# Performance work log

Hardware: AMD Instinct MI355X
Metric: run time of the kernel (lower is better)

## Reference

```python
import jax, jax.numpy as jnp
import numpy as np
from jax import lax

B, T, D = 4, 4096, 1024
H = 16                 # n_heads
HD = D // H            # head_dim = 64
NS = 64                # num_slots
SPH = NS // H          # slots_per_head = 4
KPH = 2                # effective per-head top_k = min(max(2, 32//16), 4) = 2
K = KPH * H            # total topk width = 32
HM = 4096              # hidden_mlp


def _p(key, shape, scale=0.02):
    return jax.random.normal(key, shape, dtype=jnp.float32) * scale


def setup_inputs() -> dict:
    key = jax.random.key(0)
    ks = jax.random.split(key, 24)
    return {
        "x": jax.random.normal(ks[0], (B, T, D), dtype=jnp.float32),
        "slot_init": _p(ks[1], (H, SPH, HD)),
        # route_mlp: Linear(2D, D) -> GELU -> Linear(D, NS); weights stored [in, out]
        "rw1": _p(ks[2], (2 * D, D)), "rb1": jnp.zeros((D,), jnp.float32),
        "rw2": _p(ks[3], (D, NS)), "rb2": jnp.zeros((NS,), jnp.float32),
        # GRUCell(HD, HD): torch layout [3*HD, HD]
        "gwi": _p(ks[4], (3 * HD, HD), 0.1), "gwh": _p(ks[5], (3 * HD, HD), 0.1),
        "gbi": jnp.zeros((3 * HD,), jnp.float32), "gbh": jnp.zeros((3 * HD,), jnp.float32),
        # slot_hidden_proj: Linear(HD, 4*HD); slot_out_head: Linear(4*HD, HD)
        "hpw": _p(ks[6], (HD, 4 * HD)), "hpb": jnp.zeros((4 * HD,), jnp.float32),
        "ohw": _p(ks[7], (4 * HD, HD)), "ohb": jnp.zeros((HD,), jnp.float32),
        # slot_value_proj: Linear(D, HM); slot_value_out: Linear(HM, D)
        "vpw": _p(ks[8], (D, HM)), "vpb": jnp.zeros((HM,), jnp.float32),
        "vow": _p(ks[9], (HM, D)), "vob": jnp.zeros((D,), jnp.float32),
        # out_proj: Linear(D, D)
        "opw": _p(ks[10], (D, D)), "opb": jnp.zeros((D,), jnp.float32),
        "tau": jnp.ones((1,), jnp.float32),
    }


def _gelu(x):
    return jax.nn.gelu(x, approximate=False)


def _forward(x, slot_init, rw1, rb1, rw2, rb2, gwi, gwh, gbi, gbh,
             hpw, hpb, ohw, ohb, vpw, vpb, vow, vob, opw, opb, tau):
    # ---- routing ----
    S0 = slot_init.reshape(NS, HD)                     # [NS, HD]
    slot_mean = S0.mean(axis=0)                        # [HD]
    slot_mean_full = jnp.tile(slot_mean, H)            # [D]
    ctx = jnp.concatenate(
        [x, jnp.broadcast_to(slot_mean_full, (B, T, D))], axis=-1)  # [B,T,2D]
    h1 = _gelu(ctx @ rw1 + rb1)
    route_logits = (h1 @ rw2 + rb2) / (jnp.abs(tau[0]) + 0.1)       # [B,T,NS]

    topk_vals, topk_idx = lax.top_k(route_logits, K)   # [B,T,K]
    topk_w = jax.nn.softmax(topk_vals, axis=-1)
    bi = jnp.arange(B)[:, None, None]
    ti = jnp.arange(T)[None, :, None]
    alpha = jnp.zeros((B, T, NS), x.dtype).at[bi, ti, topk_idx].set(topk_w)

    # ---- per-head slot pooling (vectorized over heads) ----
    alpha_h = alpha.reshape(B, T, H, SPH)              # [B,T,H,S]
    x_heads = x.reshape(B, T, H, HD)                   # [B,T,H,HD]
    slot_input = jnp.einsum('bths,bthd->bhsd', alpha_h, x_heads)   # [B,H,S,HD]
    wsum = alpha_h.sum(axis=1) + 1e-8                  # [B,H,S]
    slot_in = slot_input / wsum[..., None]

    # ---- GRU cell update (torch GRUCell semantics) ----
    h_prev = jnp.broadcast_to(slot_init[None], (B, H, SPH, HD))
    gi = slot_in @ gwi.T + gbi                         # [B,H,S,3HD]
    gh = h_prev @ gwh.T + gbh
    ir, iz, in_ = jnp.split(gi, 3, axis=-1)
    hr, hz, hn = jnp.split(gh, 3, axis=-1)
    r = jax.nn.sigmoid(ir + hr)
    z = jax.nn.sigmoid(iz + hz)
    n = jnp.tanh(in_ + r * hn)
    h_new = (1.0 - z) * n + z * h_prev                 # [B,H,S,HD]

    S_new = _gelu(h_new @ hpw + hpb) @ ohw + ohb       # [B,H,S,HD]

    # ---- broadcast back to tokens ----
    out = jnp.einsum('bths,bhsd->bthd', alpha_h, S_new).reshape(B, T, D)
    out = _gelu(out @ vpw + vpb) @ vow + vob
    out = out @ opw + opb
    return out


def reference(x, slot_init, rw1, rb1, rw2, rb2, gwi, gwh, gbi, gbh,
              hpw, hpb, ohw, ohb, vpw, vpb, vow, vob, opw, opb, tau):
    return _forward(x, slot_init, rw1, rb1, rw2, rb2, gwi, gwh, gbi, gbh,
                    hpw, hpb, ohw, ohb, vpw, vpb, vow, vob, opw, opb, tau)
```

## Files before the change

### kernel.cpp

```cpp
#include <hip/hip_runtime.h>
#include <cstddef>
#include <cstdint>

#define Bb 4
#define Tt 4096
#define Dd 1024
#define Hh 16
#define HDd 64
#define NSs 64
#define SPHh 4
#define HMm 4096
#define MTOK (Bb*Tt)

typedef _Float16 f16x8 __attribute__((ext_vector_type(8)));
typedef _Float16 f16x4 __attribute__((ext_vector_type(4)));
typedef float f32x4 __attribute__((ext_vector_type(4)));

__device__ __forceinline__ float gelu_f(float x) {
    return 0.5f * x * (1.0f + erff(x * 0.70710678118654752440f));
}

__device__ __forceinline__ int xcd_swz(int nwg) {
    int orig = blockIdx.y * gridDim.x + blockIdx.x;
    int cpx = nwg >> 3;
    return (orig & 7) * cpx + (orig >> 3);
}

__global__ __launch_bounds__(256) void cb_part_k(const float* __restrict__ slot_init,
                                                 const float* __restrict__ rw1,
                                                 float* __restrict__ cbp) {
    __shared__ float sm[64];
    int tid = threadIdx.x;
    if (tid < 64) {
        float s = 0.f;
        for (int i = 0; i < 64; ++i) s += slot_init[i * 64 + tid];
        sm[tid] = s * (1.0f / 64.0f);
    }
    __syncthreads();
    int j = blockIdx.x * 256 + tid;
    int k0 = blockIdx.y * 64;
    float acc = 0.f;
#pragma unroll 8
    for (int k = 0; k < 64; ++k)
        acc = fmaf(sm[k], rw1[(size_t)(1024 + k0 + k) * 1024 + j], acc);
    cbp[(size_t)blockIdx.y * 1024 + j] = acc;
}

__global__ __launch_bounds__(256) void cb_comb_k(const float* __restrict__ cbp,
                                                 float* __restrict__ cb) {
    int j = blockIdx.x * 256 + threadIdx.x;
    float acc = 0.f;
#pragma unroll
    for (int c = 0; c < 16; ++c) acc += cbp[(size_t)c * 1024 + j];
    cb[j] = acc;
}

__global__ __launch_bounds__(256) void wsplitT_k(const float* __restrict__ rw1,
                                                 _Float16* __restrict__ whiT,
                                                 _Float16* __restrict__ wloT) {
    __shared__ float t[32][33];
    int n0 = blockIdx.x * 32, k0 = blockIdx.y * 32;
    int tx = threadIdx.x & 31, ty = threadIdx.x >> 5;
#pragma unroll
    for (int i = 0; i < 32; i += 8)
        t[ty + i][tx] = rw1[(size_t)(k0 + ty + i) * 1024 + n0 + tx];
    __syncthreads();
#pragma unroll
    for (int i = 0; i < 32; i += 8) {
        float v = t[tx][ty + i];
        _Float16 h = (_Float16)v;
        _Float16 l = (_Float16)(v - (float)h);
        whiT[(size_t)(n0 + ty + i) * 1024 + k0 + tx] = h;
        wloT[(size_t)(n0 + ty + i) * 1024 + k0 + tx] = l;
    }
}

__global__ __launch_bounds__(256) void xsplit_k(const float* __restrict__ x,
                                                _Float16* __restrict__ xhi,
                                                _Float16* __restrict__ xlo) {
    size_t i = ((size_t)blockIdx.x * 256 + threadIdx.x) * 8;
    float4 a = *(const float4*)(x + i);
    float4 b = *(const float4*)(x + i + 4);
    float v[8] = {a.x, a.y, a.z, a.w, b.x, b.y, b.z, b.w};
    f16x8 h, l;
#pragma unroll
    for (int j = 0; j < 8; ++j) {
        _Float16 hv = (_Float16)v[j];
        h[j] = hv;
        l[j] = (_Float16)(v[j] - (float)hv);
    }
    *(f16x8*)(xhi + i) = h;
    *(f16x8*)(xlo + i) = l;
}

__global__ __launch_bounds__(512, 2) void hgemm4p_k(const _Float16* __restrict__ Ah,
                                                    const _Float16* __restrict__ Al,
                                                    const _Float16* __restrict__ Bh,
                                                    const _Float16* __restrict__ Bl,
                                                    const float* __restrict__ bias1,
                                                    const float* __restrict__ bias2,
                                                    float* __restrict__ C,
                                                    int M, int N, int K) {
    __shared__ __align__(16) _Float16 Ahs[2][256][32];
    __shared__ __align__(16) _Float16 Als[2][256][32];
    __shared__ __align__(16) _Float16 Bhs[2][256][32];
    __shared__ __align__(16) _Float16 Bls[2][256][32];
    const int tid = threadIdx.x;
    const int wid = tid >> 6;
    const int lane = tid & 63;
    const int swz = xcd_swz(gridDim.x * gridDim.y);
    const int brow = (swz / gridDim.x) * 256;
    const int bcol = (swz % gridDim.x) * 256;
    const int wm = wid >> 2;
    const int wn = wid & 3;

    const int srow = lane >> 2;
    const int scol = ((lane & 3) ^ ((lane >> 3) & 3)) * 8;
    const int fr = lane & 15;
    const int fkp = (((lane >> 4) ^ ((lane >> 1) & 3))) * 8;
    const int crow = (lane >> 4) * 4;

    const int nk = K >> 5;

    f32x4 acc[8][4];
#pragma unroll
    for (int m = 0; m < 8; ++m)
#pragma unroll
        for (int n = 0; n < 4; ++n)
            acc[m][n] = f32x4{0.f, 0.f, 0.f, 0.f};

    auto stage = [&](int t) {
        const int slot = t & 1;
        const size_t kk = (size_t)t << 5;
#pragma unroll
        for (int i = 0; i < 2; ++i) {
            int r0 = wid * 32 + i * 16;
            const _Float16* gah = Ah + (size_t)(brow + r0 + srow) * K + kk + scol;
            __builtin_amdgcn_global_load_lds(
                (const __attribute__((address_space(1))) void*)gah,
                (__attribute__((address_space(3))) void*)&Ahs[slot][r0][0], 16, 0, 0);
            const _Float16* gal = Al + (size_t)(brow + r0 + srow) * K + kk + scol;
            __builtin_amdgcn_global_load_lds(
                (const __attribute__((address_space(1))) void*)gal,
                (__attribute__((address_space(3))) void*)&Als[slot][r0][0], 16, 0, 0);
            const _Float16* gbh = Bh + (size_t)(bcol + r0 + srow) * K + kk + scol;
            __builtin_amdgcn_global_load_lds(
                (const __attribute__((address_space(1))) void*)gbh,
                (__attribute__((address_space(3))) void*)&Bhs[slot][r0][0], 16, 0, 0);
            const _Float16* gbl = Bl + (size_t)(bcol + r0 + srow) * K + kk + scol;
            __builtin_amdgcn_global_load_lds(
                (const __attribute__((address_space(1))) void*)gbl,
                (__attribute__((address_space(3))) void*)&Bls[slot][r0][0], 16, 0, 0);
        }
    };

    stage(0);
    if (nk > 1) stage(1);

    for (int t = 0; t < nk; ++t) {
        if (t + 1 < nk) asm volatile("s_waitcnt vmcnt(8)" ::: "memory");
        else            asm volatile("s_waitcnt vmcnt(0)" ::: "memory");
        __builtin_amdgcn_sched_barrier(0);
        __builtin_amdgcn_s_barrier();
        __builtin_amdgcn_sched_barrier(0);

        const int slot = t & 1;
        f16x8 afh[8], afl[8], bfh[4], bfl[4];
#pragma unroll
        for (int m = 0; m < 4; ++m) {
            afh[m] = *(const f16x8*)&Ahs[slot][wm * 128 + m * 16 + fr][fkp];
            afl[m] = *(const f16x8*)&Als[slot][wm * 128 + m * 16 + fr][fkp];
        }
#pragma unroll
        for (int n = 0; n < 4; ++n) {
            bfh[n] = *(const f16x8*)&Bhs[slot][wn * 64 + n * 16 + fr][fkp];
            bfl[n] = *(const f16x8*)&Bls[slot][wn * 64 + n * 16 + fr][fkp];
        }
        __builtin_amdgcn_sched_barrier(0);
        __builtin_amdgcn_s_barrier();
        asm volatile("s_waitcnt lgkmcnt(0)" ::: "memory");
        __builtin_amdgcn_sched_barrier(0);
        __builtin_amdgcn_s_setprio(1);
#pragma unroll
        for (int m = 0; m < 4; ++m)
#pragma unroll
            for (int n = 0; n < 4; ++n) {
                acc[m][n] = __builtin_amdgcn_mfma_f32_16x16x32_f16(afl[m], bfh[n], acc[m][n], 0, 0, 0);
                acc[m][n] = __builtin_amdgcn_mfma_f32_16x16x32_f16(afh[m], bfl[n], acc[m][n], 0, 0, 0);
                acc[m][n] = __builtin_amdgcn_mfma_f32_16x16x32_f16(afh[m], bfh[n], acc[m][n], 0, 0, 0);
            }
        __builtin_amdgcn_s_setprio(0);
        __builtin_amdgcn_sched_barrier(0);
#pragma unroll
        for (int m = 4; m < 8; ++m) {
            afh[m] = *(const f16x8*)&Ahs[slot][wm * 128 + m * 16 + fr][fkp];
            afl[m] = *(const f16x8*)&Als[slot][wm * 128 + m * 16 + fr][fkp];
        }
        asm volatile("s_waitcnt lgkmcnt(0)" ::: "memory");
        __builtin_amdgcn_sched_barrier(0);
        __builtin_amdgcn_s_barrier();
        __builtin_amdgcn_sched_barrier(0);
        if (t + 2 < nk) stage(t + 2);
        __builtin_amdgcn_s_setprio(1);
#pragma unroll
        for (int m = 4; m < 8; ++m)
#pragma unroll
            for (int n = 0; n < 4; ++n) {
                acc[m][n] = __builtin_amdgcn_mfma_f32_16x16x32_f16(afl[m], bfh[n], acc[m][n], 0, 0, 0);
                acc[m][n] = __builtin_amdgcn_mfma_f32_16x16x32_f16(afh[m], bfl[n], acc[m][n], 0, 0, 0);
                acc[m][n] = __builtin_amdgcn_mfma_f32_16x16x32_f16(afh[m], bfh[n], acc[m][n], 0, 0, 0);
            }
        __builtin_amdgcn_s_setprio(0);
        __builtin_amdgcn_sched_barrier(0);
    }

#pragma unroll
    for (int m = 0; m < 8; ++m) {
        int row0 = brow + wm * 128 + m * 16 + crow;
#pragma unroll
        for (int n = 0; n < 4; ++n) {
            int col = bcol + wn * 64 + n * 16 + fr;
            float bv = bias1[col] + bias2[col];
#pragma unroll
            for (int r = 0; r < 4; ++r) {
                float v = acc[m][n][r] + bv;
                C[(size_t)(row0 + r) * N + col] = gelu_f(v);
            }
        }
    }
    (void)M;
}

__global__ __launch_bounds__(256) void logits2_k(const float* __restrict__ A,
                                                 const float* __restrict__ Bw,
                                                 const float* __restrict__ rb2,
                                                 const float* __restrict__ taup,
                                                 float* __restrict__ Cl) {
    __shared__ float At[16][68];
    __shared__ float Bs[16][64];
    const int tid = threadIdx.x;
    const int m0 = blockIdx.x * 64;
    const int rg = tid >> 4;
    const int cg = tid & 15;
    const int srow = tid >> 2;
    const int skk  = (tid & 3) * 4;
    const int bk = tid >> 4;
    const int bc = (tid & 15) * 4;

    float acc[4][4] = {};

    for (int k0 = 0; k0 < 1024; k0 += 16) {
        float4 av = *(const float4*)(A + (size_t)(m0 + srow) * 1024 + k0 + skk);
        float4 bv = *(const float4*)(Bw + (size_t)(k0 + bk) * 64 + bc);
        __syncthreads();
        At[skk + 0][srow] = av.x;
        At[skk + 1][srow] = av.y;
        At[skk + 2][srow] = av.z;
        At[skk + 3][srow] = av.w;
        *(float4*)&Bs[bk][bc] = bv;
        __syncthreads();
#pragma unroll
        for (int k = 0; k < 16; ++k) {
            float4 a4 = *(const float4*)&At[k][rg * 4];
            float4 b4 = *(const float4*)&Bs[k][cg * 4];
            float a[4] = {a4.x, a4.y, a4.z, a4.w};
            float b[4] = {b4.x, b4.y, b4.z, b4.w};
#pragma unroll
            for (int i = 0; i < 4; ++i)
#pragma unroll
                for (int j = 0; j < 4; ++j)
                    acc[i][j] = fmaf(a[i], b[j], acc[i][j]);
        }
    }
    float inv = 1.0f / (fabsf(taup[0]) + 0.1f);
#pragma unroll
    for (int i = 0; i < 4; ++i)
#pragma unroll
        for (int j = 0; j < 4; ++j)
            Cl[(size_t)(m0 + rg * 4 + i) * 64 + cg * 4 + j] =
                (acc[i][j] + rb2[cg * 4 + j]) * inv;
}

__global__ __launch_bounds__(256) void topk_k(const float* __restrict__ logits,
                                              float* __restrict__ alpha,
                                              _Float16* __restrict__ alpha16) {
    int wave = threadIdx.x >> 6;
    int lane = threadIdx.x & 63;
    int t = blockIdx.x * 4 + wave;
    float li = logits[(size_t)t * 64 + lane];
    float m = li;
#pragma unroll
    for (int off = 32; off; off >>= 1) m = fmaxf(m, __shfl_xor(m, off, 64));
    int cnt = 0;
    for (int off = 1; off < 64; ++off) {
        int j = (lane + off) & 63;
        float lj = __shfl(li, j, 64);
        cnt += (lj > li) || (lj == li && j < lane);
    }
    float e = (cnt < 32) ? expf(li - m) : 0.0f;
    float s = e;
#pragma unroll
    for (int off = 32; off; off >>= 1) s += __shfl_xor(s, off, 64);
    float a = e / s;
    alpha[(size_t)t * 64 + lane] = a;
    alpha16[(size_t)t * 64 + lane] = (_Float16)a;
}

__global__ __launch_bounds__(256) void pool_part_k(const float* __restrict__ x,
                                                   const float* __restrict__ alpha,
                                                   float* __restrict__ part,
                                                   float* __restrict__ partw) {
    int bh = blockIdx.x;
    int c = blockIdx.y;
    int b = bh >> 4, h = bh & 15;
    int tid = threadIdx.x;
    int s = tid >> 6, d = tid & 63;
    __shared__ float lx[16][64];
    __shared__ float la[16][4];
    float acc = 0.f, wacc = 0.f;
    const int tchunk = Tt / 8;
    const int t0base = c * tchunk;
    for (int t0 = 0; t0 < tchunk; t0 += 16) {
        int ttr = tid >> 4;
        int ddr = (tid & 15) * 4;
        size_t trow = (size_t)b * Tt + t0base + t0 + ttr;
        float4 xv = *(const float4*)(x + trow * Dd + h * 64 + ddr);
        *(float4*)&lx[ttr][ddr] = xv;
        if (tid < 64) {
            int tt2 = tid >> 2, ss = tid & 3;
            la[tt2][ss] = alpha[((size_t)b * Tt + t0base + t0 + tt2) * 64 + h * 4 + ss];
        }
        __syncthreads();
#pragma unroll
        for (int q = 0; q < 16; ++q) {
            float av = la[q][s];
            acc = fmaf(av, lx[q][d], acc);
            wacc += av;
        }
        __syncthreads();
    }
    part[(((size_t)c * 64 + bh) * 4 + s) * 64 + d] = acc;
    if (d == 0) partw[((size_t)c * 64 + bh) * 4 + s] = wacc;
}

__global__ __launch_bounds__(256) void pool_comb_k(const float* __restrict__ part,
                                                   const float* __restrict__ partw,
                                                   float* __restrict__ slot_in) {
    int bh = blockIdx.x;
    int tid = threadIdx.x;
    int s = tid >> 6, d = tid & 63;
    float acc = 0.f, w = 0.f;
    for (int c = 0; c < 8; ++c) {
        acc += part[(((size_t)c * 64 + bh) * 4 + s) * 64 + d];
        w   += partw[((size_t)c * 64 + bh) * 4 + s];
    }
    slot_in[((size_t)bh * 4 + s) * 64 + d] = acc / (w + 1e-8f);
}

__global__ __launch_bounds__(64) void gru_k(const float* __restrict__ slot_in,
                                            const float* __restrict__ slot_init,
                                            const float* __restrict__ gwi,
                                            const float* __restrict__ gwh,
                                            const float* __restrict__ gbi,
                                            const float* __restrict__ gbh,
                                            const float* __restrict__ hpw,
                                            const float* __restrict__ hpb,
                                            const float* __restrict__ ohw,
                                            const float* __restrict__ ohb,
                                            float* __restrict__ S_new) {
    int slot = blockIdx.x;
    int hs = slot & 63;
    int d = threadIdx.x;
    __shared__ float si[64], hp[64], hn[64], g[256];
    si[d] = slot_in[(size_t)slot * 64 + d];
    hp[d] = slot_init[(size_t)hs * 64 + d];
    __syncthreads();
    float gi_r = gbi[d], gi_z = gbi[64 + d], gi_n = gbi[128 + d];
    float gh_r = gbh[d], gh_z = gbh[64 + d], gh_n = gbh[128 + d];
    for (int k = 0; k < 64; ++k) {
        float sv = si[k], hv = hp[k];
        gi_r = fmaf(sv, gwi[(size_t)(d) * 64 + k], gi_r);
        gi_z = fmaf(sv, gwi[(size_t)(64 + d) * 64 + k], gi_z);
        gi_n = fmaf(sv, gwi[(size_t)(128 + d) * 64 + k], gi_n);
        gh_r = fmaf(hv, gwh[(size_t)(d) * 64 + k], gh_r);
        gh_z = fmaf(hv, gwh[(size_t)(64 + d) * 64 + k], gh_z);
        gh_n = fmaf(hv, gwh[(size_t)(128 + d) * 64 + k], gh_n);
    }
    float r = 1.0f / (1.0f + expf(-(gi_r + gh_r)));
    float z = 1.0f / (1.0f + expf(-(gi_z + gh_z)));
    float n = tanhf(gi_n + r * gh_n);
    float hnew = (1.0f - z) * n + z * hp[d];
    hn[d] = hnew;
    __syncthreads();
    float p0 = hpb[d], p1 = hpb[64 + d], p2 = hpb[128 + d], p3 = hpb[192 + d];
    for (int k = 0; k < 64; ++k) {
        float hv = hn[k];
        p0 = fmaf(hv, hpw[(size_t)k * 256 + d], p0);
        p1 = fmaf(hv, hpw[(size_t)k * 256 + 64 + d], p1);
        p2 = fmaf(hv, hpw[(size_t)k * 256 + 128 + d], p2);
        p3 = fmaf(hv, hpw[(size_t)k * 256 + 192 + d], p3);
    }
    g[d] = gelu_f(p0); g[64 + d] = gelu_f(p1); g[128 + d] = gelu_f(p2); g[192 + d] = gelu_f(p3);
    __syncthreads();
    float o = ohb[d];
    for (int j = 0; j < 256; ++j) o = fmaf(g[j], ohw[(size_t)j * 64 + d], o);
    S_new[(size_t)slot * 64 + d] = o;
}

__global__ __launch_bounds__(256) void pmat_k(const float* __restrict__ Snew,
                                              const float* __restrict__ vpw,
                                              _Float16* __restrict__ PT) {
    const int h = blockIdx.y;
    const int tid = threadIdx.x;
    const int j = blockIdx.x * 256 + tid;
    __shared__ float S[16][64];
    for (int i = tid; i < 1024; i += 256) {
        int row = i >> 6, d = i & 63;
        int b = row >> 2, s = row & 3;
        S[row][d] = Snew[((size_t)b * 64 + h * 4 + s) * 64 + d];
    }
    __syncthreads();
    float acc[16];
#pragma unroll
    for (int r = 0; r < 16; ++r) acc[r] = 0.f;
    const float* wp = vpw + (size_t)h * 64 * HMm + j;
#pragma unroll 4
    for (int d = 0; d < 64; ++d) {
        float w = wp[(size_t)d * HMm];
#pragma unroll
        for (int r = 0; r < 16; ++r) acc[r] = fmaf(S[r][d], w, acc[r]);
    }
#pragma unroll
    for (int b = 0; b < 4; ++b) {
        f16x4 o;
#pragma unroll
        for (int s = 0; s < 4; ++s) o[s] = (_Float16)acc[b * 4 + s];
        *(f16x4*)&PT[((size_t)b * HMm + j) * 64 + h * 4] = o;
    }
}

__global__ __launch_bounds__(256) void transp_f16_k(const float* __restrict__ in,
                                                    _Float16* __restrict__ out,
                                                    int K, int N) {
    __shared__ float t[32][33];
    int n0 = blockIdx.x * 32, k0 = blockIdx.y * 32;
    int tx = threadIdx.x & 31, ty = threadIdx.x >> 5;
#pragma unroll
    for (int i = 0; i < 32; i += 8)
        t[ty + i][tx] = in[(size_t)(k0 + ty + i) * N + n0 + tx];
    __syncthreads();
#pragma unroll
    for (int i = 0; i < 32; i += 8)
        out[(size_t)(n0 + ty + i) * K + k0 + tx] = (_Float16)t[tx][ty + i];
}

__global__ __launch_bounds__(256) void vgen_k(const _Float16* __restrict__ alpha16,
                                              const _Float16* __restrict__ PT,
                                              const float* __restrict__ vpb,
                                              _Float16* __restrict__ v1a,
                                              _Float16* __restrict__ v1b) {
    __shared__ __align__(16) _Float16 As[128][64];
    __shared__ __align__(16) _Float16 Bs[128][64];
    const int tid = threadIdx.x;
    const int wid = tid >> 6;
    const int lane = tid & 63;
    const int swz = xcd_swz(gridDim.x * gridDim.y);
    const int brow = (swz / gridDim.x) * 128;
    const int bcol = (swz % gridDim.x) * 128;
    const int b = brow >> 12;
    const _Float16* Bt = PT + (size_t)b * HMm * 64;
    _Float16* Cb = (brow < 8192) ? v1a : v1b;
    const int rowoff = (brow < 8192) ? brow : brow - 8192;
    const int wr = (wid >> 1) * 64;
    const int wc = (wid & 1) * 64;

    f32x4 acc[4][4];
#pragma unroll
    for (int m = 0; m < 4; ++m)
#pragma unroll
        for (int n = 0; n < 4; ++n)
            acc[m][n] = f32x4{0.f, 0.f, 0.f, 0.f};

    const int lrow = lane >> 3;
    const int lcol = (lane & 7) * 8;
    const int fr = lane & 15;
    const int fk = (lane >> 4) * 8;

#pragma unroll
    for (int i = 0; i < 4; ++i) {
        int seg = wid * 4 + i;
        const _Float16* g = alpha16 + (size_t)(brow + seg * 8 + lrow) * 64 + lcol;
        __builtin_amdgcn_global_load_lds(
            (const __attribute__((address_space(1))) void*)g,
            (__attribute__((address_space(3))) void*)&As[seg * 8][0], 16, 0, 0);
    }
#pragma unroll
    for (int i = 0; i < 4; ++i) {
        int seg = wid * 4 + i;
        const _Float16* g = Bt + (size_t)(bcol + seg * 8 + lrow) * 64 + lcol;
        __builtin_amdgcn_global_load_lds(
            (const __attribute__((address_space(1))) void*)g,
            (__attribute__((address_space(3))) void*)&Bs[seg * 8][0], 16, 0, 0);
    }
    __syncthreads();
#pragma unroll
    for (int kb = 0; kb < 2; ++kb) {
        f16x8 af[4], bf[4];
#pragma unroll
        for (int m = 0; m < 4; ++m)
            af[m] = *(const f16x8*)&As[wr + m * 16 + fr][kb * 32 + fk];
#pragma unroll
        for (int n = 0; n < 4; ++n)
            bf[n] = *(const f16x8*)&Bs[wc + n * 16 + fr][kb * 32 + fk];
#pragma unroll
        for (int m = 0; m < 4; ++m)
#pragma unroll
            for (int n = 0; n < 4; ++n)
                acc[m][n] = __builtin_amdgcn_mfma_f32_16x16x32_f16(af[m], bf[n], acc[m][n], 0, 0, 0);
    }

    const int crow = (lane >> 4) * 4;
#pragma unroll
    for (int m = 0; m < 4; ++m) {
        int row0 = rowoff + wr + m * 16 + crow;
#pragma unroll
        for (int n = 0; n < 4; ++n) {
            int col = bcol + wc + n * 16 + fr;
            float bv = vpb[col];
#pragma unroll
            for (int r = 0; r < 4; ++r) {
                float v = acc[m][n][r] + bv;
                Cb[(size_t)(row0 + r) * HMm + col] = (_Float16)gelu_f(v);
            }
        }
    }
}

template <int OUT_F16>
__global__ __launch_bounds__(512, 2) void hgemm8_k(const _Float16* __restrict__ A0,
                                                   const _Float16* __restrict__ A1,
                                                   int splitrow,
                                                   const _Float16* __restrict__ Bt,
                                                   const float* __restrict__ bias,
                                                   void* __restrict__ Cv,
                                                   int M, int N, int K) {
    __shared__ __align__(16) _Float16 As[4][256][32];
    __shared__ __align__(16) _Float16 Bs[4][256][32];
    const int tid = threadIdx.x;
    const int wid = tid >> 6;
    const int lane = tid & 63;
    const int swz = xcd_swz(gridDim.x * gridDim.y);
    const int brow = (swz / gridDim.x) * 256;
    const int bcol = (swz % gridDim.x) * 256;
    const _Float16* Ab = (brow < splitrow) ? A0 : A1;
    const int arow0 = brow - ((brow < splitrow) ? 0 : splitrow);
    const int wm = wid >> 2;
    const int wn = wid & 3;

    const int srow = lane >> 2;
    const int scol = ((lane & 3) ^ ((lane >> 3) & 3)) * 8;
    const int fr = lane & 15;
    const int fkp = (((lane >> 4) ^ ((lane >> 1) & 3))) * 8;
    const int crow = (lane >> 4) * 4;

    const int nk = K >> 5;

    f32x4 acc[8][4];
#pragma unroll
    for (int m = 0; m < 8; ++m)
#pragma unroll
        for (int n = 0; n < 4; ++n)
            acc[m][n] = f32x4{0.f, 0.f, 0.f, 0.f};

    auto stage = [&](int t) {
        const int slot = t & 3;
        const size_t kk = (size_t)t << 5;
#pragma unroll
        for (int i = 0; i < 2; ++i) {
            const _Float16* g = Ab + (size_t)(arow0 + wid * 32 + i * 16 + srow) * K + kk + scol;
            __builtin_amdgcn_global_load_lds(
                (const __attribute__((address_space(1))) void*)g,
                (__attribute__((address_space(3))) void*)&As[slot][wid * 32 + i * 16][0], 16, 0, 0);
        }
#pragma unroll
        for (int i = 0; i < 2; ++i) {
            const _Float16* g = Bt + (size_t)(bcol + wid * 32 + i * 16 + srow) * K + kk + scol;
            __builtin_amdgcn_global_load_lds(
                (const __attribute__((address_space(1))) void*)g,
                (__attribute__((address_space(3))) void*)&Bs[slot][wid * 32 + i * 16][0], 16, 0, 0);
        }
    };

    stage(0);
    if (nk > 1) stage(1);
    if (nk > 2) stage(2);

    for (int t = 0; t < nk; ++t) {
        if (t + 2 < nk)      asm volatile("s_waitcnt vmcnt(8)" ::: "memory");
        else if (t + 1 < nk) asm volatile("s_waitcnt vmcnt(4)" ::: "memory");
        else                 asm volatile("s_waitcnt vmcnt(0)" ::: "memory");
        __builtin_amdgcn_sched_barrier(0);
        __builtin_amdgcn_s_barrier();
        __builtin_amdgcn_sched_barrier(0);

        const int slot = t & 3;
        f16x8 af[8], bf[4];
#pragma unroll
        for (int m = 0; m < 4; ++m)
            af[m] = *(const f16x8*)&As[slot][wm * 128 + m * 16 + fr][fkp];
#pragma unroll
        for (int n = 0; n < 4; ++n)
            bf[n] = *(const f16x8*)&Bs[slot][wn * 64 + n * 16 + fr][fkp];
        if (t + 3 < nk) stage(t + 3);
        __builtin_amdgcn_sched_barrier(0);
        __builtin_amdgcn_s_barrier();
        asm volatile("s_waitcnt lgkmcnt(0)" ::: "memory");
        __builtin_amdgcn_sched_barrier(0);
        __builtin_amdgcn_s_setprio(1);
#pragma unroll
        for (int m = 0; m < 4; ++m)
#pragma unroll
            for (int n = 0; n < 4; ++n)
                acc[m][n] = __builtin_amdgcn_mfma_f32_16x16x32_f16(af[m], bf[n], acc[m][n], 0, 0, 0);
        __builtin_amdgcn_s_setprio(0);
        __builtin_amdgcn_sched_barrier(0);
#pragma unroll
        for (int m = 4; m < 8; ++m)
            af[m] = *(const f16x8*)&As[slot][wm * 128 + m * 16 + fr][fkp];
        __builtin_amdgcn_sched_barrier(0);
        __builtin_amdgcn_s_barrier();
        asm volatile("s_waitcnt lgkmcnt(0)" ::: "memory");
        __builtin_amdgcn_sched_barrier(0);
        __builtin_amdgcn_s_setprio(1);
#pragma unroll
        for (int m = 4; m < 8; ++m)
#pragma unroll
            for (int n = 0; n < 4; ++n)
                acc[m][n] = __builtin_amdgcn_mfma_f32_16x16x32_f16(af[m], bf[n], acc[m][n], 0, 0, 0);
        __builtin_amdgcn_s_setprio(0);
        __builtin_amdgcn_sched_barrier(0);
    }

#pragma unroll
    for (int m = 0; m < 8; ++m) {
        int row0 = brow + wm * 128 + m * 16 + crow;
#pragma unroll
        for (int n = 0; n < 4; ++n) {
            int col = bcol + wn * 64 + n * 16 + fr;
            float bv = bias[col];
#pragma unroll
            for (int r = 0; r < 4; ++r) {
                float v = acc[m][n][r] + bv;
                size_t idx = (size_t)(row0 + r) * N + col;
                if (OUT_F16) ((_Float16*)Cv)[idx] = (_Float16)v;
                else ((float*)Cv)[idx] = v;
            }
        }
    }
    (void)M;
}

extern "C" void kernel_launch(void* const* d_in, const int* in_sizes, int n_in,
                              void* d_out, int out_size, void* d_ws, size_t ws_size,
                              hipStream_t stream) {
    const float* x         = (const float*)d_in[0];
    const float* slot_init = (const float*)d_in[1];
    const float* rw1       = (const float*)d_in[2];
    const float* rb1       = (const float*)d_in[3];
    const float* rw2       = (const float*)d_in[4];
    const float* rb2       = (const float*)d_in[5];
    const float* gwi       = (const float*)d_in[6];
    const float* gwh       = (const float*)d_in[7];
    const float* gbi       = (const float*)d_in[8];
    const float* gbh       = (const float*)d_in[9];
    const float* hpw       = (const float*)d_in[10];
    const float* hpb       = (const float*)d_in[11];
    const float* ohw       = (const float*)d_in[12];
    const float* ohb       = (const float*)d_in[13];
    const float* vpw       = (const float*)d_in[14];
    const float* vpb       = (const float*)d_in[15];
    const float* vow       = (const float*)d_in[16];
    const float* vob       = (const float*)d_in[17];
    const float* opw       = (const float*)d_in[18];
    const float* opb       = (const float*)d_in[19];
    const float* tau       = (const float*)d_in[20];
    float* out = (float*)d_out;

    float* ws = (float*)d_ws;
    size_t off = 0;
    auto alloc = [&](size_t nfloats) { float* p = ws + off; off += (nfloats + 63) & ~(size_t)63; return p; };

    float* cb     = alloc(1024);
    float* cbp    = alloc(16 * 1024);
    float* h1     = alloc((size_t)MTOK * 1024);
    _Float16* v1a = (_Float16*)h1;
    float* logits = alloc((size_t)MTOK * 64);
    float* alpha  = alloc((size_t)MTOK * 64);
    _Float16* alpha16 = (_Float16*)alloc((size_t)MTOK * 64 / 2);
    float* slotin = alloc(256 * 64);
    float* part   = alloc((size_t)8 * 64 * 4 * 64);
    float* partw  = alloc(8 * 64 * 4);
    float* Snew   = alloc(256 * 64);
    _Float16* PT   = (_Float16*)alloc((size_t)Bb * HMm * 64 / 2);
    _Float16* vowT = (_Float16*)alloc((size_t)Dd * HMm / 2);
    _Float16* opwT = (_Float16*)alloc((size_t)Dd * Dd / 2);
    _Float16* v2f16 = (_Float16*)alloc((size_t)MTOK * Dd / 2);
    _Float16* w1hiT = (_Float16*)alloc((size_t)Dd * Dd / 2);
    _Float16* w1loT = (_Float16*)alloc((size_t)Dd * Dd / 2);

    _Float16* xhi = (_Float16*)d_out;
    _Float16* xlo = xhi + (size_t)MTOK * Dd;
    _Float16* v1b = (_Float16*)d_out;

    cb_part_k<<<dim3(4, 16), 256, 0, stream>>>(slot_init, rw1, cbp);
    cb_comb_k<<<4, 256, 0, stream>>>(cbp, cb);
    wsplitT_k<<<dim3(Dd / 32, Dd / 32), 256, 0, stream>>>(rw1, w1hiT, w1loT);
    xsplit_k<<<(MTOK * Dd) / (256 * 8), 256, 0, stream>>>(x, xhi, xlo);
    hgemm4p_k<<<dim3(Dd / 256, MTOK / 256), 512, 0, stream>>>(
        xhi, xlo, w1hiT, w1loT, rb1, cb, h1, MTOK, Dd, Dd);
    logits2_k<<<MTOK / 64, 256, 0, stream>>>(h1, rw2, rb2, tau, logits);
    topk_k<<<MTOK / 4, 256, 0, stream>>>(logits, alpha, alpha16);

    transp_f16_k<<<dim3(Dd / 32, HMm / 32), 256, 0, stream>>>(vow, vowT, HMm, Dd);
    transp_f16_k<<<dim3(Dd / 32, Dd / 32), 256, 0, stream>>>(opw, opwT, Dd, Dd);

    pool_part_k<<<dim3(64, 8), 256, 0, stream>>>(x, alpha, part, partw);
    pool_comb_k<<<64, 256, 0, stream>>>(part, partw, slotin);
    gru_k<<<256, 64, 0, stream>>>(slotin, slot_init, gwi, gwh, gbi, gbh,
                                  hpw, hpb, ohw, ohb, Snew);

    pmat_k<<<dim3(HMm / 256, Hh), 256, 0, stream>>>(Snew, vpw, PT);

    vgen_k<<<dim3(HMm / 128, MTOK / 128), 256, 0, stream>>>(
        alpha16, PT, vpb, v1a, v1b);
    hgemm8_k<1><<<dim3(Dd / 256, MTOK / 256), 512, 0, stream>>>(
        v1a, v1b, 8192, vowT, vob, v2f16, MTOK, Dd, HMm);
    hgemm8_k<0><<<dim3(Dd / 256, MTOK / 256), 512, 0, stream>>>(
        v2f16, v2f16, MTOK, opwT, opb, out, MTOK, Dd, Dd);

    (void)in_sizes; (void)n_in; (void)out_size; (void)ws_size;
}
```

Baseline: 545.8 us.

## Use BK=64 double-buffered LDS pipeline with four-phase MFMA ping-pong in hgemm8

Changes the hgemm8 kernel from a 4-slot BK=32 ring buffer to a 2-slot BK=64 double buffer with a wider 8-way XOR swizzle. The inner loop is split into four MFMA phases over quadrants of the 256x256 tile, interleaving fragment loads between them, and the next stage is issued only after a barrier late in the iteration. The aim is fewer barriers and waitcnts per unit of K work and larger MFMA bursts between syncs. The trade-off is a shallower prefetch depth (one tile ahead instead of two), which may expose global-load latency.

```diff
diff --git a/kernel.cpp b/kernel.cpp
--- a/kernel.cpp
+++ b/kernel.cpp
@@ -544,8 +544,8 @@
                                                    const float* __restrict__ bias,
                                                    void* __restrict__ Cv,
                                                    int M, int N, int K) {
-    __shared__ __align__(16) _Float16 As[4][256][32];
-    __shared__ __align__(16) _Float16 Bs[4][256][32];
+    __shared__ __align__(16) _Float16 As[2][256][64];
+    __shared__ __align__(16) _Float16 Bs[2][256][64];
     const int tid = threadIdx.x;
     const int wid = tid >> 6;
     const int lane = tid & 63;
@@ -557,13 +557,14 @@
     const int wm = wid >> 2;
     const int wn = wid & 3;
 
-    const int srow = lane >> 2;
-    const int scol = ((lane & 3) ^ ((lane >> 3) & 3)) * 8;
+    const int srow = lane >> 3;
+    const int scol = ((lane & 7) ^ (lane >> 3)) * 8;
     const int fr = lane & 15;
-    const int fkp = (((lane >> 4) ^ ((lane >> 1) & 3))) * 8;
+    const int fk0 = (((lane >> 4) ^ (lane & 7))) * 8;
+    const int fk1 = (((4 + (lane >> 4)) ^ (lane & 7))) * 8;
     const int crow = (lane >> 4) * 4;
 
-    const int nk = K >> 5;
+    const int nk = K >> 6;
 
     f32x4 acc[8][4];
 #pragma unroll
@@ -573,45 +574,46 @@
             acc[m][n] = f32x4{0.f, 0.f, 0.f, 0.f};
 
     auto stage = [&](int t) {
-        const int slot = t & 3;
-        const size_t kk = (size_t)t << 5;
-#pragma unroll
-        for (int i = 0; i < 2; ++i) {
-            const _Float16* g = Ab + (size_t)(arow0 + wid * 32 + i * 16 + srow) * K + kk + scol;
+        const int slot = t & 1;
+        const size_t kk = (size_t)t << 6;
+#pragma unroll
+        for (int j = 0; j < 4; ++j) {
+            const _Float16* ga = Ab + (size_t)(arow0 + j * 64 + wid * 8 + srow) * K + kk + scol;
             __builtin_amdgcn_global_load_lds(
-                (const __attribute__((address_space(1))) void*)g,
-                (__attribute__((address_space(3))) void*)&As[slot][wid * 32 + i * 16][0], 16, 0, 0);
-        }
-#pragma unroll
-        for (int i = 0; i < 2; ++i) {
-            const _Float16* g = Bt + (size_t)(bcol + wid * 32 + i * 16 + srow) * K + kk + scol;
+                (const __attribute__((address_space(1))) void*)ga,
+                (__attribute__((address_space(3))) void*)&As[slot][j * 64 + wid * 8][0], 16, 0, 0);
+        }
+#pragma unroll
+        for (int j = 0; j < 4; ++j) {
+            const _Float16* gb = Bt + (size_t)(bcol + j * 64 + wid * 8 + srow) * K + kk + scol;
             __builtin_amdgcn_global_load_lds(
-                (const __attribute__((address_space(1))) void*)g,
-                (__attribute__((address_space(3))) void*)&Bs[slot][wid * 32 + i * 16][0], 16, 0, 0);
+                (const __attribute__((address_space(1))) void*)gb,
+                (__attribute__((address_space(3))) void*)&Bs[slot][j * 64 + wid * 8][0], 16, 0, 0);
         }
     };
 
     stage(0);
-    if (nk > 1) stage(1);
-    if (nk > 2) stage(2);
+    stage(1);
 
     for (int t = 0; t < nk; ++t) {
-        if (t + 2 < nk)      asm volatile("s_waitcnt vmcnt(8)" ::: "memory");
-        else if (t + 1 < nk) asm volatile("s_waitcnt vmcnt(4)" ::: "memory");
-        else                 asm volatile("s_waitcnt vmcnt(0)" ::: "memory");
+        if (t + 1 < nk) asm volatile("s_waitcnt vmcnt(8)" ::: "memory");
+        else            asm volatile("s_waitcnt vmcnt(0)" ::: "memory");
         __builtin_amdgcn_sched_barrier(0);
         __builtin_amdgcn_s_barrier();
         __builtin_amdgcn_sched_barrier(0);
 
-        const int slot = t & 3;
-        f16x8 af[8], bf[4];
-#pragma unroll
-        for (int m = 0; m < 4; ++m)
-            af[m] = *(const f16x8*)&As[slot][wm * 128 + m * 16 + fr][fkp];
-#pragma unroll
-        for (int n = 0; n < 4; ++n)
-            bf[n] = *(const f16x8*)&Bs[slot][wn * 64 + n * 16 + fr][fkp];
-        if (t + 3 < nk) stage(t + 3);
+        const int slot = t & 1;
+        f16x8 af[4][2], bf[4][2];
+#pragma unroll
+        for (int m = 0; m < 4; ++m) {
+            af[m][0] = *(const f16x8*)&As[slot][wm * 128 + m * 16 + fr][fk0];
+            af[m][1] = *(const f16x8*)&As[slot][wm * 128 + m * 16 + fr][fk1];
+        }
+#pragma unroll
+        for (int n = 0; n < 2; ++n) {
+            bf[n][0] = *(const f16x8*)&Bs[slot][wn * 64 + n * 16 + fr][fk0];
+            bf[n][1] = *(const f16x8*)&Bs[slot][wn * 64 + n * 16 + fr][fk1];
+        }
         __builtin_amdgcn_sched_barrier(0);
         __builtin_amdgcn_s_barrier();
         asm volatile("s_waitcnt lgkmcnt(0)" ::: "memory");
@@ -620,23 +622,61 @@
 #pragma unroll
         for (int m = 0; m < 4; ++m)
 #pragma unroll
-            for (int n = 0; n < 4; ++n)
-                acc[m][n] = __builtin_amdgcn_mfma_f32_16x16x32_f16(af[m], bf[n], acc[m][n], 0, 0, 0);
+            for (int n = 0; n < 2; ++n)
+#pragma unroll
+                for (int kk = 0; kk < 2; ++kk)
+                    acc[m][n] = __builtin_amdgcn_mfma_f32_16x16x32_f16(af[m][kk], bf[n][kk], acc[m][n], 0, 0, 0);
         __builtin_amdgcn_s_setprio(0);
         __builtin_amdgcn_sched_barrier(0);
 #pragma unroll
-        for (int m = 4; m < 8; ++m)
-            af[m] = *(const f16x8*)&As[slot][wm * 128 + m * 16 + fr][fkp];
+        for (int n = 2; n < 4; ++n) {
+            bf[n][0] = *(const f16x8*)&Bs[slot][wn * 64 + n * 16 + fr][fk0];
+            bf[n][1] = *(const f16x8*)&Bs[slot][wn * 64 + n * 16 + fr][fk1];
+        }
         __builtin_amdgcn_sched_barrier(0);
         __builtin_amdgcn_s_barrier();
         asm volatile("s_waitcnt lgkmcnt(0)" ::: "memory");
         __builtin_amdgcn_sched_barrier(0);
         __builtin_amdgcn_s_setprio(1);
 #pragma unroll
-        for (int m = 4; m < 8; ++m)
-#pragma unroll
-            for (int n = 0; n < 4; ++n)
-                acc[m][n] = __builtin_amdgcn_mfma_f32_16x16x32_f16(af[m], bf[n], acc[m][n], 0, 0, 0);
+        for (int m = 0; m < 4; ++m)
+#pragma unroll
+            for (int n = 2; n < 4; ++n)
+#pragma unroll
+                for (int kk = 0; kk < 2; ++kk)
+                    acc[m][n] = __builtin_amdgcn_mfma_f32_16x16x32_f16(af[m][kk], bf[n][kk], acc[m][n], 0, 0, 0);
+        __builtin_amdgcn_s_setprio(0);
+        __builtin_amdgcn_sched_barrier(0);
+#pragma unroll
+        for (int m = 0; m < 4; ++m) {
+            af[m][0] = *(const f16x8*)&As[slot][wm * 128 + (m + 4) * 16 + fr][fk0];
+            af[m][1] = *(const f16x8*)&As[slot][wm * 128 + (m + 4) * 16 + fr][fk1];
+        }
+        __builtin_amdgcn_sched_barrier(0);
+        __builtin_amdgcn_s_barrier();
+        asm volatile("s_waitcnt lgkmcnt(0)" ::: "memory");
+        __builtin_amdgcn_sched_barrier(0);
+        __builtin_amdgcn_s_setprio(1);
+#pragma unroll
+        for (int m = 0; m < 4; ++m)
+#pragma unroll
+            for (int n = 0; n < 2; ++n)
+#pragma unroll
+                for (int kk = 0; kk < 2; ++kk)
+                    acc[m + 4][n] = __builtin_amdgcn_mfma_f32_16x16x32_f16(af[m][kk], bf[n][kk], acc[m + 4][n], 0, 0, 0);
+        __builtin_amdgcn_s_setprio(0);
+        __builtin_amdgcn_sched_barrier(0);
+        __builtin_amdgcn_s_barrier();
+        __builtin_amdgcn_sched_barrier(0);
+        if (t + 2 < nk) stage(t + 2);
+        __builtin_amdgcn_s_setprio(1);
+#pragma unroll
+        for (int m = 0; m < 4; ++m)
+#pragma unroll
+            for (int n = 2; n < 4; ++n)
+#pragma unroll
+                for (int kk = 0; kk < 2; ++kk)
+                    acc[m + 4][n] = __builtin_amdgcn_mfma_f32_16x16x32_f16(af[m][kk], bf[n][kk], acc[m + 4][n], 0, 0, 0);
         __builtin_amdgcn_s_setprio(0);
         __builtin_amdgcn_sched_barrier(0);
     }
```

New measurement: 521.3 us. 1.05x faster.
